# Optimization experiments

Hardware: AMD Instinct MI355X
Metric: run time of the kernel (lower is better)

The kernel has to match this reference:

```python
import jax, jax.numpy as jnp
import numpy as np

B, D, K = 32768, 1024, 64
N3, N4, N5 = 512, 512, 512


def setup_inputs() -> dict:
    key = jax.random.key(0)
    ks = jax.random.split(key, 10)
    # x in [-1, 1]^D as the docstring states
    x = jax.random.uniform(ks[0], (B, D), dtype=jnp.float32, minval=-1.0, maxval=1.0)
    S = jnp.sort(jax.random.randint(ks[1], (K,), 0, D, dtype=jnp.int32))
    a = jax.random.normal(ks[2], (K,), dtype=jnp.float32)
    b = jax.random.normal(ks[3], (K, K), dtype=jnp.float32)
    idx3 = jax.random.randint(ks[4], (N3, 3), 0, K, dtype=jnp.int32)
    c3 = jax.random.normal(ks[5], (N3,), dtype=jnp.float32)
    idx4 = jax.random.randint(ks[6], (N4, 4), 0, K, dtype=jnp.int32)
    c4 = jax.random.normal(ks[7], (N4,), dtype=jnp.float32)
    idx5 = jax.random.randint(ks[8], (N5, 5), 0, K, dtype=jnp.int32)
    c5 = jax.random.normal(ks[9], (N5,), dtype=jnp.float32)
    return {"x": x, "S": S, "a": a, "b": b, "idx3": idx3, "c3": c3,
            "idx4": idx4, "c4": c4, "idx5": idx5, "c5": c5}


def _monomial_term(xS, idx, c):
    # xS: (B,k); idx: (n,deg); c: (n,) -> (B,)
    # gather -> (B, n, deg), product over monomial factors, weighted sum
    prod = jnp.prod(xS[:, idx], axis=2)  # (B, n)
    return prod @ c


def reference(x, S, a, b, idx3, c3, idx4, c4, idx5, c5):
    xS = x[:, S]                      # (B, k)
    lin = xS @ a                      # (B,)
    # sum_{i<j} b[i,j] xS_i xS_j == einsum with strictly-upper-triangular b
    bu = jnp.triu(b, k=1)             # (k, k)
    quad = jnp.einsum('bi,ij,bj->b', xS, bu, xS)
    out = lin + quad
    out = out + _monomial_term(xS, idx3, c3)
    out = out + _monomial_term(xS, idx4, c4)
    out = out + _monomial_term(xS, idx5, c5)
    return out
```

## Files before the change

kernel.cpp:

```cpp
#include <hip/hip_runtime.h>
#include <stdint.h>

#define NT 256
#define RPB 64
#define XSTR_B 272

#define WS_BU   0
#define WS_P3   16384
#define WS_P4   24576
#define WS_C4   32768
#define WS_P5   34816
#define WS_P5B  43008

static __device__ __forceinline__ float4 f4fma(float s, float4 v, float4 acc) {
    acc.x += s * v.x; acc.y += s * v.y; acc.z += s * v.z; acc.w += s * v.w;
    return acc;
}

__global__ void prepack_kernel(const float* __restrict__ b,
                               const int* __restrict__ i3, const float* __restrict__ c3,
                               const int* __restrict__ i4, const float* __restrict__ c4,
                               const int* __restrict__ i5, const float* __restrict__ c5,
                               unsigned char* __restrict__ ws)
{
    const int g = blockIdx.x * NT + threadIdx.x;
    const int stride = gridDim.x * NT;
    float* bu  = (float*)(ws + WS_BU);
    uint4* p3  = (uint4*)(ws + WS_P3);
    uint4* p4  = (uint4*)(ws + WS_P4);
    float* c4o = (float*)(ws + WS_C4);
    uint4* p5  = (uint4*)(ws + WS_P5);
    uint2* p5b = (uint2*)(ws + WS_P5B);

    for (int e = g; e < 4096; e += stride) {
        int i = e >> 6, j = e & 63;
        bu[e] = (i < j) ? b[e] : 0.0f;
    }
    for (int t = g; t < 512; t += stride) {
        p3[t] = make_uint4((unsigned)i3[3*t+0] * XSTR_B, (unsigned)i3[3*t+1] * XSTR_B,
                           (unsigned)i3[3*t+2] * XSTR_B, __float_as_uint(c3[t]));
        p4[t] = make_uint4((unsigned)i4[4*t+0] * XSTR_B, (unsigned)i4[4*t+1] * XSTR_B,
                           (unsigned)i4[4*t+2] * XSTR_B, (unsigned)i4[4*t+3] * XSTR_B);
        c4o[t] = c4[t];
        p5[t] = make_uint4((unsigned)i5[5*t+0] * XSTR_B, (unsigned)i5[5*t+1] * XSTR_B,
                           (unsigned)i5[5*t+2] * XSTR_B, (unsigned)i5[5*t+3] * XSTR_B);
        p5b[t] = make_uint2((unsigned)i5[5*t+4] * XSTR_B, __float_as_uint(c5[t]));
    }
}

__global__ __launch_bounds__(NT, 2)
void poly_main(const float* __restrict__ x, const int* __restrict__ S,
               const float* __restrict__ a,
               const unsigned char* __restrict__ ws,
               float* __restrict__ out)
{
    __shared__ float xS[64 * 68];
    __shared__ float bS[64 * 64];
    __shared__ float aS[64];
    __shared__ short slot[1024];
    __shared__ short lead[64];
    __shared__ float red[1024];

    const int tid  = threadIdx.x;
    const int row0 = blockIdx.x * RPB;

    ((short4*)slot)[tid] = make_short4(-1, -1, -1, -1);
    {
        const float4* bin = (const float4*)(ws + WS_BU);
        float4* bsh = (float4*)bS;
        #pragma unroll
        for (int m = 0; m < 4; ++m) bsh[tid + m * NT] = bin[tid + m * NT];
    }
    if (tid < 64) aS[tid] = a[tid];
    __syncthreads();
    if (tid < 64) {
        int sv = S[tid];
        int k0 = tid;
        while (k0 > 0 && S[k0 - 1] == sv) --k0;
        lead[tid] = (short)k0;
        if (k0 == tid) slot[sv] = (short)tid;
    }
    __syncthreads();

    {
        short4 sl = ((short4*)slot)[tid];
        int o0 = (int)sl.x * XSTR_B;
        int o1 = (int)sl.y * XSTR_B;
        int o2 = (int)sl.z * XSTR_B;
        int o3 = (int)sl.w * XSTR_B;
        const float4* Xrow = (const float4*)(x + (size_t)row0 * 1024);
        char* xsb = (char*)xS;
        #pragma unroll 4
        for (int r = 0; r < RPB; ++r) {
            float4 v = Xrow[r * 256 + tid];
            int rb = r * 4;
            if (sl.x >= 0) *(float*)(xsb + o0 + rb) = v.x;
            if (sl.y >= 0) *(float*)(xsb + o1 + rb) = v.y;
            if (sl.z >= 0) *(float*)(xsb + o2 + rb) = v.z;
            if (sl.w >= 0) *(float*)(xsb + o3 + rb) = v.w;
        }
    }
    __syncthreads();

    {
        int k = tid >> 2, q = tid & 3;
        int k0 = lead[k];
        if (k0 != k) {
            float4* dst = (float4*)((char*)xS + k  * XSTR_B) + q * 4;
            const float4* src = (const float4*)((char*)xS + k0 * XSTR_B) + q * 4;
            #pragma unroll
            for (int m = 0; m < 4; ++m) dst[m] = src[m];
        }
    }
    __syncthreads();

    const int rg = tid & 15;
    const int ts = tid >> 4;
    const char* xb = (const char*)xS + rg * 16;

    float4 d0 = make_float4(0.f, 0.f, 0.f, 0.f);
    float4 d1 = d0, d2 = d0, d3 = d0;
    #pragma unroll 8
    for (int i = 0; i < 64; ++i) {
        float4 xi = *(const float4*)(xb + i * XSTR_B);
        float b0 = bS[i * 64 + ts];
        float b1 = bS[i * 64 + ts + 16];
        float b2 = bS[i * 64 + ts + 32];
        float b3 = bS[i * 64 + ts + 48];
        d0 = f4fma(b0, xi, d0);
        d1 = f4fma(b1, xi, d1);
        d2 = f4fma(b2, xi, d2);
        d3 = f4fma(b3, xi, d3);
    }
    float4 xj0 = *(const float4*)(xb + (ts +  0) * XSTR_B);
    float4 xj1 = *(const float4*)(xb + (ts + 16) * XSTR_B);
    float4 xj2 = *(const float4*)(xb + (ts + 32) * XSTR_B);
    float4 xj3 = *(const float4*)(xb + (ts + 48) * XSTR_B);
    float a0 = aS[ts], a1 = aS[ts + 16], a2 = aS[ts + 32], a3 = aS[ts + 48];

    float4 acc;
    acc.x = (a0 + d0.x) * xj0.x + (a1 + d1.x) * xj1.x + (a2 + d2.x) * xj2.x + (a3 + d3.x) * xj3.x;
    acc.y = (a0 + d0.y) * xj0.y + (a1 + d1.y) * xj1.y + (a2 + d2.y) * xj2.y + (a3 + d3.y) * xj3.y;
    acc.z = (a0 + d0.z) * xj0.z + (a1 + d1.z) * xj1.z + (a2 + d2.z) * xj2.z + (a3 + d3.z) * xj3.z;
    acc.w = (a0 + d0.w) * xj0.w + (a1 + d1.w) * xj1.w + (a2 + d2.w) * xj2.w + (a3 + d3.w) * xj3.w;

    const uint4* p3g  = (const uint4*)(ws + WS_P3);
    const uint4* p4g  = (const uint4*)(ws + WS_P4);
    const float* c4g  = (const float*)(ws + WS_C4);
    const uint4* p5g  = (const uint4*)(ws + WS_P5);
    const uint2* p5bg = (const uint2*)(ws + WS_P5B);

    #pragma unroll 2
    for (int m = 0; m < 32; ++m) {
        uint4 p = p3g[16 * m + ts];
        float4 v0 = *(const float4*)(xb + p.x);
        float4 v1 = *(const float4*)(xb + p.y);
        float4 v2 = *(const float4*)(xb + p.z);
        float c = __uint_as_float(p.w);
        acc.x += c * (v0.x * v1.x * v2.x);
        acc.y += c * (v0.y * v1.y * v2.y);
        acc.z += c * (v0.z * v1.z * v2.z);
        acc.w += c * (v0.w * v1.w * v2.w);
    }
    #pragma unroll 2
    for (int m = 0; m < 32; ++m) {
        uint4 p = p4g[16 * m + ts];
        float c = c4g[16 * m + ts];
        float4 v0 = *(const float4*)(xb + p.x);
        float4 v1 = *(const float4*)(xb + p.y);
        float4 v2 = *(const float4*)(xb + p.z);
        float4 v3 = *(const float4*)(xb + p.w);
        acc.x += c * ((v0.x * v1.x) * (v2.x * v3.x));
        acc.y += c * ((v0.y * v1.y) * (v2.y * v3.y));
        acc.z += c * ((v0.z * v1.z) * (v2.z * v3.z));
        acc.w += c * ((v0.w * v1.w) * (v2.w * v3.w));
    }
    #pragma unroll 2
    for (int m = 0; m < 32; ++m) {
        uint4 p = p5g[16 * m + ts];
        uint2 q = p5bg[16 * m + ts];
        float4 v0 = *(const float4*)(xb + p.x);
        float4 v1 = *(const float4*)(xb + p.y);
        float4 v2 = *(const float4*)(xb + p.z);
        float4 v3 = *(const float4*)(xb + p.w);
        float4 v4 = *(const float4*)(xb + q.x);
        float c = __uint_as_float(q.y);
        acc.x += c * (((v0.x * v1.x) * (v2.x * v3.x)) * v4.x);
        acc.y += c * (((v0.y * v1.y) * (v2.y * v3.y)) * v4.y);
        acc.z += c * (((v0.z * v1.z) * (v2.z * v3.z)) * v4.z);
        acc.w += c * (((v0.w * v1.w) * (v2.w * v3.w)) * v4.w);
    }

    ((float4*)red)[ts * 16 + rg] = acc;
    __syncthreads();
    if (tid < 64) {
        float s = 0.f;
        #pragma unroll
        for (int t = 0; t < 16; ++t) s += red[t * 64 + tid];
        out[row0 + tid] = s;
    }
}

extern "C" void kernel_launch(void* const* d_in, const int* in_sizes, int n_in,
                              void* d_out, int out_size, void* d_ws, size_t ws_size,
                              hipStream_t stream) {
    const float* x  = (const float*)d_in[0];
    const int*   S  = (const int*)d_in[1];
    const float* a  = (const float*)d_in[2];
    const float* b  = (const float*)d_in[3];
    const int*   i3 = (const int*)d_in[4];
    const float* c3 = (const float*)d_in[5];
    const int*   i4 = (const int*)d_in[6];
    const float* c4 = (const float*)d_in[7];
    const int*   i5 = (const int*)d_in[8];
    const float* c5 = (const float*)d_in[9];
    unsigned char* ws = (unsigned char*)d_ws;
    float* out = (float*)d_out;

    prepack_kernel<<<16, NT, 0, stream>>>(b, i3, c3, i4, c4, i5, c5, ws);
    poly_main<<<32768 / RPB, NT, 0, stream>>>(x, S, a, ws, out);
}
```

Before: 236.8 us.

## Double threads per block, halve per-thread monomial and quadratic work

```diff
diff --git a/kernel.cpp b/kernel.cpp
--- a/kernel.cpp
+++ b/kernel.cpp
@@ -1,11 +1,11 @@
 #include <hip/hip_runtime.h>
 #include <stdint.h>
 
-#define NT 256
+#define NT 512
 #define RPB 64
 #define XSTR_B 272
 
-#define WS_BU   0
+#define WS_BU2  0
 #define WS_P3   16384
 #define WS_P4   24576
 #define WS_C4   32768
@@ -23,18 +23,20 @@
                                const int* __restrict__ i5, const float* __restrict__ c5,
                                unsigned char* __restrict__ ws)
 {
-    const int g = blockIdx.x * NT + threadIdx.x;
-    const int stride = gridDim.x * NT;
-    float* bu  = (float*)(ws + WS_BU);
+    const int g = blockIdx.x * 256 + threadIdx.x;
+    const int stride = gridDim.x * 256;
+    float2* bu2 = (float2*)(ws + WS_BU2);
     uint4* p3  = (uint4*)(ws + WS_P3);
     uint4* p4  = (uint4*)(ws + WS_P4);
     float* c4o = (float*)(ws + WS_C4);
     uint4* p5  = (uint4*)(ws + WS_P5);
     uint2* p5b = (uint2*)(ws + WS_P5B);
 
-    for (int e = g; e < 4096; e += stride) {
-        int i = e >> 6, j = e & 63;
-        bu[e] = (i < j) ? b[e] : 0.0f;
+    for (int e = g; e < 2048; e += stride) {
+        int i = e >> 5, j = e & 31;
+        float lo = (i < j)      ? b[i * 64 + j]      : 0.0f;
+        float hi = (i < j + 32) ? b[i * 64 + j + 32] : 0.0f;
+        bu2[e] = make_float2(lo, hi);
     }
     for (int t = g; t < 512; t += stride) {
         p3[t] = make_uint4((unsigned)i3[3*t+0] * XSTR_B, (unsigned)i3[3*t+1] * XSTR_B,
@@ -48,28 +50,28 @@
     }
 }
 
-__global__ __launch_bounds__(NT, 2)
+__global__ __launch_bounds__(NT, 4)
 void poly_main(const float* __restrict__ x, const int* __restrict__ S,
                const float* __restrict__ a,
                const unsigned char* __restrict__ ws,
                float* __restrict__ out)
 {
-    __shared__ float xS[64 * 68];
-    __shared__ float bS[64 * 64];
-    __shared__ float aS[64];
-    __shared__ short slot[1024];
-    __shared__ short lead[64];
-    __shared__ float red[1024];
+    __shared__ float  xS[64 * 68];
+    __shared__ float2 buS[64 * 32];
+    __shared__ float  aS[64];
+    __shared__ short  slot[1024];
+    __shared__ short  lead[64];
+    __shared__ float  red[32 * 64];
 
     const int tid  = threadIdx.x;
     const int row0 = blockIdx.x * RPB;
 
-    ((short4*)slot)[tid] = make_short4(-1, -1, -1, -1);
+    if (tid < 256) ((short4*)slot)[tid] = make_short4(-1, -1, -1, -1);
     {
-        const float4* bin = (const float4*)(ws + WS_BU);
-        float4* bsh = (float4*)bS;
-        #pragma unroll
-        for (int m = 0; m < 4; ++m) bsh[tid + m * NT] = bin[tid + m * NT];
+        const float4* bin = (const float4*)(ws + WS_BU2);
+        float4* bsh = (float4*)buS;
+        bsh[tid]       = bin[tid];
+        bsh[tid + 512] = bin[tid + 512];
     }
     if (tid < 64) aS[tid] = a[tid];
     __syncthreads();
@@ -83,26 +85,32 @@
     __syncthreads();
 
     {
-        short4 sl = ((short4*)slot)[tid];
-        int o0 = (int)sl.x * XSTR_B;
-        int o1 = (int)sl.y * XSTR_B;
-        int o2 = (int)sl.z * XSTR_B;
-        int o3 = (int)sl.w * XSTR_B;
-        const float4* Xrow = (const float4*)(x + (size_t)row0 * 1024);
-        char* xsb = (char*)xS;
-        #pragma unroll 4
-        for (int r = 0; r < RPB; ++r) {
-            float4 v = Xrow[r * 256 + tid];
-            int rb = r * 4;
-            if (sl.x >= 0) *(float*)(xsb + o0 + rb) = v.x;
-            if (sl.y >= 0) *(float*)(xsb + o1 + rb) = v.y;
-            if (sl.z >= 0) *(float*)(xsb + o2 + rb) = v.z;
-            if (sl.w >= 0) *(float*)(xsb + o3 + rb) = v.w;
+        const int col4 = tid & 255;
+        const int r0   = tid >> 8;
+        short4 sl = ((short4*)slot)[col4];
+        short mx = max(max(sl.x, sl.y), max(sl.z, sl.w));
+        if (mx >= 0) {
+            int o0 = (int)sl.x * XSTR_B;
+            int o1 = (int)sl.y * XSTR_B;
+            int o2 = (int)sl.z * XSTR_B;
+            int o3 = (int)sl.w * XSTR_B;
+            const float4* Xrow = (const float4*)(x + (size_t)row0 * 1024);
+            char* xsb = (char*)xS;
+            #pragma unroll 4
+            for (int it = 0; it < 32; ++it) {
+                int r = r0 + it * 2;
+                float4 v = Xrow[r * 256 + col4];
+                int rb = r * 4;
+                if (sl.x >= 0) *(float*)(xsb + o0 + rb) = v.x;
+                if (sl.y >= 0) *(float*)(xsb + o1 + rb) = v.y;
+                if (sl.z >= 0) *(float*)(xsb + o2 + rb) = v.z;
+                if (sl.w >= 0) *(float*)(xsb + o3 + rb) = v.w;
+            }
         }
     }
     __syncthreads();
 
-    {
+    if (tid < 256) {
         int k = tid >> 2, q = tid & 3;
         int k0 = lead[k];
         if (k0 != k) {
@@ -119,30 +127,23 @@
     const char* xb = (const char*)xS + rg * 16;
 
     float4 d0 = make_float4(0.f, 0.f, 0.f, 0.f);
-    float4 d1 = d0, d2 = d0, d3 = d0;
+    float4 d1 = d0;
     #pragma unroll 8
     for (int i = 0; i < 64; ++i) {
         float4 xi = *(const float4*)(xb + i * XSTR_B);
-        float b0 = bS[i * 64 + ts];
-        float b1 = bS[i * 64 + ts + 16];
-        float b2 = bS[i * 64 + ts + 32];
-        float b3 = bS[i * 64 + ts + 48];
-        d0 = f4fma(b0, xi, d0);
-        d1 = f4fma(b1, xi, d1);
-        d2 = f4fma(b2, xi, d2);
-        d3 = f4fma(b3, xi, d3);
-    }
-    float4 xj0 = *(const float4*)(xb + (ts +  0) * XSTR_B);
-    float4 xj1 = *(const float4*)(xb + (ts + 16) * XSTR_B);
-    float4 xj2 = *(const float4*)(xb + (ts + 32) * XSTR_B);
-    float4 xj3 = *(const float4*)(xb + (ts + 48) * XSTR_B);
-    float a0 = aS[ts], a1 = aS[ts + 16], a2 = aS[ts + 32], a3 = aS[ts + 48];
+        float2 bb = buS[i * 32 + ts];
+        d0 = f4fma(bb.x, xi, d0);
+        d1 = f4fma(bb.y, xi, d1);
+    }
+    float4 xj0 = *(const float4*)(xb + ts * XSTR_B);
+    float4 xj1 = *(const float4*)(xb + (ts + 32) * XSTR_B);
+    float a0 = aS[ts], a1 = aS[ts + 32];
 
     float4 acc;
-    acc.x = (a0 + d0.x) * xj0.x + (a1 + d1.x) * xj1.x + (a2 + d2.x) * xj2.x + (a3 + d3.x) * xj3.x;
-    acc.y = (a0 + d0.y) * xj0.y + (a1 + d1.y) * xj1.y + (a2 + d2.y) * xj2.y + (a3 + d3.y) * xj3.y;
-    acc.z = (a0 + d0.z) * xj0.z + (a1 + d1.z) * xj1.z + (a2 + d2.z) * xj2.z + (a3 + d3.z) * xj3.z;
-    acc.w = (a0 + d0.w) * xj0.w + (a1 + d1.w) * xj1.w + (a2 + d2.w) * xj2.w + (a3 + d3.w) * xj3.w;
+    acc.x = (a0 + d0.x) * xj0.x + (a1 + d1.x) * xj1.x;
+    acc.y = (a0 + d0.y) * xj0.y + (a1 + d1.y) * xj1.y;
+    acc.z = (a0 + d0.z) * xj0.z + (a1 + d1.z) * xj1.z;
+    acc.w = (a0 + d0.w) * xj0.w + (a1 + d1.w) * xj1.w;
 
     const uint4* p3g  = (const uint4*)(ws + WS_P3);
     const uint4* p4g  = (const uint4*)(ws + WS_P4);
@@ -150,9 +151,9 @@
     const uint4* p5g  = (const uint4*)(ws + WS_P5);
     const uint2* p5bg = (const uint2*)(ws + WS_P5B);
 
-    #pragma unroll 2
-    for (int m = 0; m < 32; ++m) {
-        uint4 p = p3g[16 * m + ts];
+    #pragma unroll 4
+    for (int m = 0; m < 16; ++m) {
+        uint4 p = p3g[32 * m + ts];
         float4 v0 = *(const float4*)(xb + p.x);
         float4 v1 = *(const float4*)(xb + p.y);
         float4 v2 = *(const float4*)(xb + p.z);
@@ -162,10 +163,10 @@
         acc.z += c * (v0.z * v1.z * v2.z);
         acc.w += c * (v0.w * v1.w * v2.w);
     }
-    #pragma unroll 2
-    for (int m = 0; m < 32; ++m) {
-        uint4 p = p4g[16 * m + ts];
-        float c = c4g[16 * m + ts];
+    #pragma unroll 4
+    for (int m = 0; m < 16; ++m) {
+        uint4 p = p4g[32 * m + ts];
+        float c = c4g[32 * m + ts];
         float4 v0 = *(const float4*)(xb + p.x);
         float4 v1 = *(const float4*)(xb + p.y);
         float4 v2 = *(const float4*)(xb + p.z);
@@ -175,10 +176,10 @@
         acc.z += c * ((v0.z * v1.z) * (v2.z * v3.z));
         acc.w += c * ((v0.w * v1.w) * (v2.w * v3.w));
     }
-    #pragma unroll 2
-    for (int m = 0; m < 32; ++m) {
-        uint4 p = p5g[16 * m + ts];
-        uint2 q = p5bg[16 * m + ts];
+    #pragma unroll 4
+    for (int m = 0; m < 16; ++m) {
+        uint4 p = p5g[32 * m + ts];
+        uint2 q = p5bg[32 * m + ts];
         float4 v0 = *(const float4*)(xb + p.x);
         float4 v1 = *(const float4*)(xb + p.y);
         float4 v2 = *(const float4*)(xb + p.z);
@@ -196,7 +197,7 @@
     if (tid < 64) {
         float s = 0.f;
         #pragma unroll
-        for (int t = 0; t < 16; ++t) s += red[t * 64 + tid];
+        for (int t = 0; t < 32; ++t) s += red[t * 64 + tid];
         out[row0 + tid] = s;
     }
 }
@@ -217,6 +218,6 @@
     unsigned char* ws = (unsigned char*)d_ws;
     float* out = (float*)d_out;
 
-    prepack_kernel<<<16, NT, 0, stream>>>(b, i3, c3, i4, c4, i5, c5, ws);
+    prepack_kernel<<<16, 256, 0, stream>>>(b, i3, c3, i4, c4, i5, c5, ws);
     poly_main<<<32768 / RPB, NT, 0, stream>>>(x, S, a, ws, out);
 }
```

New measurement: 218.8 us. -7.6%, faster.
